# Kernel optimization log

Hardware: AMD Instinct MI355X
Metric: run time of the kernel (lower is better)

Reference implementation:

```python
import jax, jax.numpy as jnp
import numpy as np

C = 512
GROUPS = 32
EPS = 1e-6


def setup_inputs() -> dict:
    key = jax.random.key(0)
    ks = jax.random.split(key, 10)
    B, H, W = 4, 64, 64
    s = 1.0 / np.sqrt(C)
    return {
        "x": jax.random.normal(ks[0], (B, C, H, W), dtype=jnp.float32),
        "gn_weight": jnp.ones((C,), jnp.float32),
        "gn_bias": jnp.zeros((C,), jnp.float32),
        "Wq": jax.random.normal(ks[1], (C, C), jnp.float32) * s,
        "bq": jnp.zeros((C,), jnp.float32),
        "Wk": jax.random.normal(ks[2], (C, C), jnp.float32) * s,
        "bk": jnp.zeros((C,), jnp.float32),
        "Wv": jax.random.normal(ks[3], (C, C), jnp.float32) * s,
        "bv": jnp.zeros((C,), jnp.float32),
        "Wo": jax.random.normal(ks[4], (C, C), jnp.float32) * s,
        "bo": jnp.zeros((C,), jnp.float32),
    }


def _group_norm(x, weight, bias):
    B, Ch, H, W = x.shape
    xg = x.reshape(B, GROUPS, Ch // GROUPS, H, W)
    mean = jnp.mean(xg, axis=(2, 3, 4), keepdims=True)
    var = jnp.var(xg, axis=(2, 3, 4), keepdims=True)
    xg = (xg - mean) * jax.lax.rsqrt(var + EPS)
    h = xg.reshape(B, Ch, H, W)
    return h * weight[None, :, None, None] + bias[None, :, None, None]


def reference(x, gn_weight, gn_bias, Wq, bq, Wk, bk, Wv, bv, Wo, bo):
    B, Ch, H, W = x.shape
    h = _group_norm(x, gn_weight, gn_bias)
    # [B, N, C] with N = H*W spatial tokens
    h = h.reshape(B, Ch, H * W).transpose(0, 2, 1)
    q = h @ Wq.T + bq
    k = h @ Wk.T + bk
    v = h @ Wv.T + bv
    scale = 1.0 / jnp.sqrt(jnp.asarray(Ch, x.dtype))
    scores = jnp.einsum("bnc,bmc->bnm", q, k) * scale  # [B, N, N]
    attn = jax.nn.softmax(scores, axis=-1)
    out = jnp.einsum("bnm,bmc->bnc", attn, v)
    out = out @ Wo.T + bo  # Dropout(0.0) is identity
    out = out.transpose(0, 2, 1).reshape(B, Ch, H, W)
    return x + out
```

## Files before the change

kernel.cpp:

```cpp
#include <hip/hip_runtime.h>
#include <hip/hip_bf16.h>

typedef __attribute__((ext_vector_type(8))) short bf16x8;
typedef __attribute__((ext_vector_type(4))) short bf16x4;
typedef __attribute__((ext_vector_type(4))) float f32x4;

__device__ __forceinline__ short f2bf(float f){
  __hip_bfloat16 h = __float2bfloat16(f);
  return __builtin_bit_cast(short, h);
}
__device__ __forceinline__ float bf2f(short s){
  unsigned u = ((unsigned)(unsigned short)s) << 16;
  return __builtin_bit_cast(float, u);
}

__device__ __forceinline__ void gload_lds16(const short* g, char* l){
  __builtin_amdgcn_global_load_lds(
      (const __attribute__((address_space(1))) void*)g,
      (__attribute__((address_space(3))) void*)l, 16, 0, 0);
}

#define SB0() __builtin_amdgcn_sched_barrier(0)

__global__ __launch_bounds__(256) void gn_stats(const float* __restrict__ x,
                                                float* __restrict__ stats){
  int b = blockIdx.x >> 5, g = blockIdx.x & 31;
  const float4* p = (const float4*)(x + ((long long)b*512 + g*16)*4096);
  float s = 0.f, s2 = 0.f;
  for (int i = threadIdx.x; i < 16384; i += 256){
    float4 v = p[i];
    s  += v.x + v.y + v.z + v.w;
    s2 += v.x*v.x + v.y*v.y + v.z*v.z + v.w*v.w;
  }
  #pragma unroll
  for (int o = 32; o; o >>= 1){ s += __shfl_xor(s, o); s2 += __shfl_xor(s2, o); }
  __shared__ float rs[4], rs2[4];
  int wid = threadIdx.x >> 6;
  if ((threadIdx.x & 63) == 0){ rs[wid] = s; rs2[wid] = s2; }
  __syncthreads();
  if (threadIdx.x == 0){
    float S  = rs[0]+rs[1]+rs[2]+rs[3];
    float S2 = rs2[0]+rs2[1]+rs2[2]+rs2[3];
    float mean = S * (1.f/65536.f);
    float var  = S2 * (1.f/65536.f) - mean*mean;
    stats[blockIdx.x*2]   = mean;
    stats[blockIdx.x*2+1] = rsqrtf(var + 1e-6f);
  }
}

__global__ __launch_bounds__(256) void gn_apply(const float* __restrict__ x,
                                                const float* __restrict__ stats,
                                                const float* __restrict__ gw,
                                                const float* __restrict__ gb,
                                                short* __restrict__ h){
  __shared__ float tile[128][65];
  int b  = blockIdx.y;
  int n0 = blockIdx.x * 64;
  int t  = threadIdx.x;
  const float* xb = x + (long long)b*512*4096;
  for (int cc = 0; cc < 4; cc++){
    int c0 = cc*128;
    #pragma unroll
    for (int r = 0; r < 128; r += 4){
      int c = r + (t >> 6);
      tile[c][t & 63] = xb[(long long)(c0+c)*4096 + n0 + (t & 63)];
    }
    __syncthreads();
    int n = t >> 2, cp = (t & 3)*32;
    short tmp[32];
    #pragma unroll
    for (int j = 0; j < 32; j++){
      int c = c0 + cp + j;
      float mean = stats[(b*32 + (c >> 4))*2];
      float rstd = stats[(b*32 + (c >> 4))*2 + 1];
      float v = (tile[cp+j][n] - mean)*rstd*gw[c] + gb[c];
      tmp[j] = f2bf(v);
    }
    long long ho = ((long long)b*4096 + n0 + n)*512 + c0 + cp;
    #pragma unroll
    for (int j2 = 0; j2 < 4; j2++){
      bf16x8 v8;
      #pragma unroll
      for (int e = 0; e < 8; e++) v8[e] = tmp[j2*8 + e];
      *(bf16x8*)&h[ho + j2*8] = v8;
    }
    __syncthreads();
  }
}

__global__ __launch_bounds__(256) void f2bf_all(
    const float* __restrict__ w0, const float* __restrict__ w1,
    const float* __restrict__ w2, const float* __restrict__ w3,
    short* __restrict__ o0, short* __restrict__ o1,
    short* __restrict__ o2, short* __restrict__ o3){
  int idx = blockIdx.x*256 + threadIdx.x;
  int m = idx >> 15, r = idx & 32767;
  const float* src = (m==0) ? w0 : (m==1) ? w1 : (m==2) ? w2 : w3;
  short* dst       = (m==0) ? o0 : (m==1) ? o1 : (m==2) ? o2 : o3;
  const float4* p = (const float4*)src + (long long)r*2;
  float4 a = p[0], c = p[1];
  bf16x8 v;
  v[0]=f2bf(a.x); v[1]=f2bf(a.y); v[2]=f2bf(a.z); v[3]=f2bf(a.w);
  v[4]=f2bf(c.x); v[5]=f2bf(c.y); v[6]=f2bf(c.z); v[7]=f2bf(c.w);
  *(bf16x8*)&dst[(long long)r*8] = v;
}

__global__ __launch_bounds__(256) void bcat(const float* __restrict__ bq,
                                            const float* __restrict__ bk,
                                            const float* __restrict__ bv,
                                            float* __restrict__ o){
  int t = blockIdx.x*256 + threadIdx.x;
  if (t < 512){ o[t] = bq[t]; o[512+t] = bk[t]; o[1024+t] = bv[t]; }
}

__global__ __launch_bounds__(256) void reduce_den(const float* __restrict__ partial,
                                                  float* __restrict__ inv_den,
                                                  int nrows){
  int r = blockIdx.x*256 + threadIdx.x;
  if (r >= nrows) return;
  const float4* p = (const float4*)(partial + (long long)r*16);
  float4 a = p[0], b = p[1], c = p[2], d = p[3];
  float s = a.x+a.y+a.z+a.w + b.x+b.y+b.z+b.w + c.x+c.y+c.z+c.w + d.x+d.y+d.z+d.w;
  inv_den[r] = 1.f / s;
}

__global__ __launch_bounds__(512, 2) void gemm8(
    const short* __restrict__ A, const short* __restrict__ Bw,
    short* __restrict__ outp,
    int Nn, int Kd,
    long long sA, long long sB, long long sO,
    float* __restrict__ partial)
{
  constexpr int BUFSZ = 65536;
  extern __shared__ char smem[];

  int id = blockIdx.x;
  int xcd = id & 7, s = id >> 3;
  int region = xcd + ((s >> 4) << 3);
  int o = s & 15;
  const int bz = region >> 4;
  const int bx = (region & 3)*4 + (o & 3);
  const int by = ((region >> 2) & 3)*4 + (o >> 2);

  const short* Ab = A + bz*sA;
  const short* Bb = Bw + bz*sB;
  const int m0 = bx*256, n0 = by*256;
  const int t = threadIdx.x;
  const int lane = t & 63, wid = t >> 6;
  const int g = lane >> 4, lr = lane & 15;
  const int wr = wid >> 2, wc = wid & 3;
  const long long KdLL = Kd;

  auto STG = [&](int kt, int buf, int which){
    const bool isB = which >= 2;
    const int h = which & 1;
    char* d = smem + buf*BUFSZ + (isB ? 32768 : 0) + h*16384 + t*16;
    const short* src = isB ? Bb : Ab;
    const int base = isB ? n0 : m0;
    #pragma unroll
    for (int p = 0; p < 2; p++){
      int row = h*128 + p*64 + (t >> 3);
      int ch = t & 7;
      gload_lds16(src + (long long)(base+row)*KdLL + (long long)kt*64 + ((ch ^ (row&7))*8),
                  d + p*8192);
    }
  };

  int roA[8], swA[8], roB[4], swB[4];
  #pragma unroll
  for (int mf = 0; mf < 8; mf++){
    int ra = wr*128 + mf*16 + lr;
    roA[mf] = ra*128; swA[mf] = ra & 7;
  }
  #pragma unroll
  for (int nf = 0; nf < 4; nf++){
    int rb = wc*64 + nf*16 + lr;
    roB[nf] = 32768 + rb*128; swB[nf] = rb & 7;
  }

  f32x4 acc[8][4];
  #pragma unroll
  for (int i = 0; i < 8; i++)
    #pragma unroll
    for (int j = 0; j < 4; j++)
      acc[i][j] = f32x4{0.f,0.f,0.f,0.f};

  bf16x8 av[4][2], bv[4][2];

  #define RD_A(QM, BASE)                                                   \
    _Pragma("unroll")                                                      \
    for (int _i = 0; _i < 4; _i++)                                         \
      _Pragma("unroll")                                                    \
      for (int _ks = 0; _ks < 2; _ks++)                                    \
        av[_i][_ks] = *(const bf16x8*)((BASE) + roA[(QM)*4+_i] +           \
                       (((_ks*4+g) ^ swA[(QM)*4+_i])<<4));
  #define RD_B(QN, BASE)                                                   \
    _Pragma("unroll")                                                      \
    for (int _j = 0; _j < 2; _j++)                                         \
      _Pragma("unroll")                                                    \
      for (int _ks = 0; _ks < 2; _ks++)                                    \
        bv[(QN)*2+_j][_ks] = *(const bf16x8*)((BASE) + roB[(QN)*2+_j] +    \
                       (((_ks*4+g) ^ swB[(QN)*2+_j])<<4));
  #define MFMA16(QN)                                                       \
    __builtin_amdgcn_s_setprio(1);                                         \
    _Pragma("unroll")                                                      \
    for (int _ks = 0; _ks < 2; _ks++)                                      \
      _Pragma("unroll")                                                    \
      for (int _m = 0; _m < 4; _m++)                                       \
        _Pragma("unroll")                                                  \
        for (int _j = 0; _j < 2; _j++)                                     \
          accp[_m][(QN)*2+_j] = __builtin_amdgcn_mfma_f32_16x16x32_bf16(   \
            bv[(QN)*2+_j][_ks], av[_m][_ks], accp[_m][(QN)*2+_j], 0,0,0);  \
    __builtin_amdgcn_s_setprio(0);

  #define LGKM0() asm volatile("s_waitcnt lgkmcnt(0)" ::: "memory")
  #define LGKM8() asm volatile("s_waitcnt lgkmcnt(8)" ::: "memory")
  #define VM4()   asm volatile("s_waitcnt vmcnt(4)" ::: "memory")
  #define VM0()   asm volatile("s_waitcnt vmcnt(0)" ::: "memory")
  #define BAR()   __builtin_amdgcn_s_barrier()

  const int NT = Kd >> 6;
  const int NI = NT >> 1;

  STG(0,0,0); STG(0,0,1); STG(0,0,2); STG(0,0,3);
  STG(1,1,2); STG(1,1,3);
  VM4();
  BAR();

  for (int i = 0; i < NI; ++i){
    const int kt0 = 2*i, kt1 = kt0 + 1;
    char* bc = smem + (kt0 & 1)*BUFSZ;
    char* bn = smem + (kt1 & 1)*BUFSZ;
    {
      f32x4 (&accp)[8][4] = acc;
      RD_A(0, bc); RD_B(0, bc);
      if (kt1 < NT) STG(kt1, kt1 & 1, 0);
      LGKM8();
      BAR();
      LGKM0();
      { f32x4 (&accp2)[8][4] = acc; (void)accp2; }
      __builtin_amdgcn_s_setprio(1);
      #pragma unroll
      for (int _ks = 0; _ks < 2; _ks++)
        #pragma unroll
        for (int _m = 0; _m < 4; _m++)
          #pragma unroll
          for (int _j = 0; _j < 2; _j++)
            acc[_m][_j] = __builtin_amdgcn_mfma_f32_16x16x32_bf16(
              bv[_j][_ks], av[_m][_ks], acc[_m][_j], 0,0,0);
      __builtin_amdgcn_s_setprio(0);
      BAR();
      RD_B(1, bc);
      if (kt1 < NT) STG(kt1, kt1 & 1, 1);
      BAR();
      LGKM0();
      __builtin_amdgcn_s_setprio(1);
      #pragma unroll
      for (int _ks = 0; _ks < 2; _ks++)
        #pragma unroll
        for (int _m = 0; _m < 4; _m++)
          #pragma unroll
          for (int _j = 2; _j < 4; _j++)
            acc[_m][_j] = __builtin_amdgcn_mfma_f32_16x16x32_bf16(
              bv[_j][_ks], av[_m][_ks], acc[_m][_j], 0,0,0);
      __builtin_amdgcn_s_setprio(0);
      BAR();
      RD_A(1, bc);
      if (kt0+2 < NT) STG(kt0+2, kt0 & 1, 2);
      BAR();
      LGKM0();
      __builtin_amdgcn_s_setprio(1);
      #pragma unroll
      for (int _ks = 0; _ks < 2; _ks++)
        #pragma unroll
        for (int _m = 0; _m < 4; _m++)
          #pragma unroll
          for (int _j = 0; _j < 2; _j++)
            acc[4+_m][_j] = __builtin_amdgcn_mfma_f32_16x16x32_bf16(
              bv[_j][_ks], av[_m][_ks], acc[4+_m][_j], 0,0,0);
      __builtin_amdgcn_s_setprio(0);
      BAR();
      if (kt0+2 < NT) STG(kt0+2, kt0 & 1, 3);
      BAR();
      __builtin_amdgcn_s_setprio(1);
      #pragma unroll
      for (int _ks = 0; _ks < 2; _ks++)
        #pragma unroll
        for (int _m = 0; _m < 4; _m++)
          #pragma unroll
          for (int _j = 2; _j < 4; _j++)
            acc[4+_m][_j] = __builtin_amdgcn_mfma_f32_16x16x32_bf16(
              bv[_j][_ks], av[_m][_ks], acc[4+_m][_j], 0,0,0);
      __builtin_amdgcn_s_setprio(0);
      if (kt1 < NT) VM4(); else VM0();
      BAR();
    }
    if (kt1 < NT){
      RD_A(0, bn); RD_B(0, bn);
      if (kt0+2 < NT) STG(kt0+2, kt0 & 1, 0);
      LGKM8();
      BAR();
      LGKM0();
      __builtin_amdgcn_s_setprio(1);
      #pragma unroll
      for (int _ks = 0; _ks < 2; _ks++)
        #pragma unroll
        for (int _m = 0; _m < 4; _m++)
          #pragma unroll
          for (int _j = 0; _j < 2; _j++)
            acc[_m][_j] = __builtin_amdgcn_mfma_f32_16x16x32_bf16(
              bv[_j][_ks], av[_m][_ks], acc[_m][_j], 0,0,0);
      __builtin_amdgcn_s_setprio(0);
      BAR();
      RD_B(1, bn);
      if (kt0+2 < NT) STG(kt0+2, kt0 & 1, 1);
      BAR();
      LGKM0();
      __builtin_amdgcn_s_setprio(1);
      #pragma unroll
      for (int _ks = 0; _ks < 2; _ks++)
        #pragma unroll
        for (int _m = 0; _m < 4; _m++)
          #pragma unroll
          for (int _j = 2; _j < 4; _j++)
            acc[_m][_j] = __builtin_amdgcn_mfma_f32_16x16x32_bf16(
              bv[_j][_ks], av[_m][_ks], acc[_m][_j], 0,0,0);
      __builtin_amdgcn_s_setprio(0);
      BAR();
      RD_A(1, bn);
      if (kt1+2 < NT) STG(kt1+2, kt1 & 1, 2);
      BAR();
      LGKM0();
      __builtin_amdgcn_s_setprio(1);
      #pragma unroll
      for (int _ks = 0; _ks < 2; _ks++)
        #pragma unroll
        for (int _m = 0; _m < 4; _m++)
          #pragma unroll
          for (int _j = 0; _j < 2; _j++)
            acc[4+_m][_j] = __builtin_amdgcn_mfma_f32_16x16x32_bf16(
              bv[_j][_ks], av[_m][_ks], acc[4+_m][_j], 0,0,0);
      __builtin_amdgcn_s_setprio(0);
      BAR();
      if (kt1+2 < NT) STG(kt1+2, kt1 & 1, 3);
      BAR();
      __builtin_amdgcn_s_setprio(1);
      #pragma unroll
      for (int _ks = 0; _ks < 2; _ks++)
        #pragma unroll
        for (int _m = 0; _m < 4; _m++)
          #pragma unroll
          for (int _j = 2; _j < 4; _j++)
            acc[4+_m][_j] = __builtin_amdgcn_mfma_f32_16x16x32_bf16(
              bv[_j][_ks], av[_m][_ks], acc[4+_m][_j], 0,0,0);
      __builtin_amdgcn_s_setprio(0);
      if (kt1+2 < NT) VM4(); else VM0();
      BAR();
    }
  }

  short* outb = outp + bz*sO;
  float* rowpart = (float*)smem;
  constexpr float LOG2E = 1.4426950408889634f;
  #pragma unroll
  for (int mi = 0; mi < 8; mi++){
    int lrow = wr*128 + mi*16 + lr;
    int row  = m0 + lrow;
    float rs = 0.f;
    #pragma unroll
    for (int ni = 0; ni < 4; ni++){
      int col = n0 + wc*64 + ni*16 + g*4;
      bf16x4 pk;
      #pragma unroll
      for (int i2 = 0; i2 < 4; i2++){
        float p = exp2f(acc[mi][ni][i2]*LOG2E);
        rs += p;
        pk[i2] = f2bf(p);
      }
      *(bf16x4*)&outb[(long long)row*Nn + col] = pk;
    }
    rs += __shfl_xor(rs, 16);
    rs += __shfl_xor(rs, 32);
    if (g == 0) rowpart[lrow*4 + wc] = rs;
  }
  __syncthreads();
  if (t < 256){
    float s2 = rowpart[t*4] + rowpart[t*4+1] + rowpart[t*4+2] + rowpart[t*4+3];
    partial[((long long)bz*4096 + m0 + t)*16 + by] = s2;
  }
  #undef RD_A
  #undef RD_B
  #undef MFMA16
  #undef LGKM0
  #undef LGKM8
  #undef VM4
  #undef VM0
  #undef BAR
}

template<int MODE, int TM, int BN, int TH, int SWZ>
__global__ __launch_bounds__(TH, 2) void gemmF(
    const short* __restrict__ A, const short* __restrict__ Bw,
    const float* __restrict__ bias,
    void* __restrict__ outp, const float* __restrict__ resid,
    int M, int Nn, int Kd,
    long long sA, long long sB, long long sO, float scale,
    const float* __restrict__ dptr, float* __restrict__ partial)
{
  constexpr int WAVES   = TH/64;
  constexpr int WARPS_N = BN/64;
  constexpr int WARPS_M = WAVES/WARPS_N;
  constexpr int WM = TM/WARPS_M;
  constexpr int MF = WM/16;
  constexpr int ABYT = TM*128;
  constexpr int BUFSZ = (TM+BN)*128;
  constexpr int APASS = (TM*128)/(TH*16);
  constexpr int BPASS = (BN*128)/(TH*16);
  constexpr int LOADS = APASS + BPASS;
  extern __shared__ char smem[];

  int bx, by, bz;
  if constexpr (SWZ == 2){
    int id = blockIdx.x;
    int xcd = id & 7, s = id >> 3;
    int combo = xcd*2 + (s & 1);
    by = combo & 3; bz = combo >> 2;
    bx = s >> 1;
  } else { bx = blockIdx.x; by = blockIdx.y; bz = blockIdx.z; }

  const short* Ab = A + bz*sA;
  const short* Bb = Bw + bz*sB;
  const int m0 = bx*TM, n0 = by*BN;
  const int t = threadIdx.x;
  const int lane = t & 63, wid = t >> 6;
  const int g = lane >> 4, lr = lane & 15;
  const int wr = wid / WARPS_N, wc = wid % WARPS_N;
  const long long KdLL = Kd;

  auto STAGE = [&](int kt, int buf){
    char* d0 = smem + buf*BUFSZ;
    #pragma unroll
    for (int p = 0; p < APASS; p++){
      int f = p*TH*16 + t*16;
      int row = f >> 7, ch = (f >> 4) & 7;
      gload_lds16(Ab + (long long)(m0+row)*KdLL + (long long)kt*64 + ((ch ^ (row&7))*8),
                  d0 + f);
    }
    #pragma unroll
    for (int p = 0; p < BPASS; p++){
      int f = p*TH*16 + t*16;
      int row = f >> 7, ch = (f >> 4) & 7;
      gload_lds16(Bb + (long long)(n0+row)*KdLL + (long long)kt*64 + ((ch ^ (row&7))*8),
                  d0 + ABYT + f);
    }
  };

  int roA[MF], swA[MF], roB[4], swB[4];
  #pragma unroll
  for (int mf = 0; mf < MF; mf++){
    int ra = wr*WM + mf*16 + lr;
    roA[mf] = ra*128; swA[mf] = ra & 7;
  }
  #pragma unroll
  for (int nf = 0; nf < 4; nf++){
    int rb = wc*64 + nf*16 + lr;
    roB[nf] = ABYT + rb*128; swB[nf] = rb & 7;
  }

  f32x4 acc[MF][4];
  #pragma unroll
  for (int i = 0; i < MF; i++)
    #pragma unroll
    for (int j = 0; j < 4; j++)
      acc[i][j] = f32x4{0.f,0.f,0.f,0.f};

  const int NT = Kd >> 6;

  STAGE(0, 0);
  STAGE(1, 1);
  if constexpr (LOADS == 8) asm volatile("s_waitcnt vmcnt(8)":::"memory");
  else                      asm volatile("s_waitcnt vmcnt(6)":::"memory");
  SB0();
  __builtin_amdgcn_s_barrier();

  for (int kt = 0; kt < NT; ++kt){
    char* base = smem + (kt & 1)*BUFSZ;
    bf16x8 av[MF][2], bv[4][2];
    #pragma unroll
    for (int n = 0; n < 4; n++)
      #pragma unroll
      for (int ks = 0; ks < 2; ks++)
        bv[n][ks] = *(const bf16x8*)(base + roB[n] + (((ks*4+g) ^ swB[n])<<4));
    #pragma unroll
    for (int m = 0; m < MF; m++)
      #pragma unroll
      for (int ks = 0; ks < 2; ks++)
        av[m][ks] = *(const bf16x8*)(base + roA[m] + (((ks*4+g) ^ swA[m])<<4));
    #pragma unroll
    for (int ks = 0; ks < 2; ks++)
      #pragma unroll
      for (int m = 0; m < MF; m++)
        #pragma unroll
        for (int n = 0; n < 4; n++){
          if constexpr (MODE == 2)
            acc[m][n] = __builtin_amdgcn_mfma_f32_16x16x32_bf16(av[m][ks], bv[n][ks], acc[m][n], 0,0,0);
          else
            acc[m][n] = __builtin_amdgcn_mfma_f32_16x16x32_bf16(bv[n][ks], av[m][ks], acc[m][n], 0,0,0);
        }
    SB0();
    __builtin_amdgcn_s_barrier();
    SB0();
    if (kt + 2 < NT){
      STAGE(kt + 2, kt & 1);
      if constexpr (LOADS == 8) asm volatile("s_waitcnt vmcnt(8)":::"memory");
      else                      asm volatile("s_waitcnt vmcnt(6)":::"memory");
    } else {
      asm volatile("s_waitcnt vmcnt(0)":::"memory");
    }
    __builtin_amdgcn_s_barrier();
  }

  if constexpr (MODE == 4){
    short* outb = (short*)outp + bz*sO;
    float* rowpart = (float*)smem;
    constexpr float LOG2E = 1.4426950408889634f;
    #pragma unroll
    for (int mi = 0; mi < MF; mi++){
      int lrow = wr*WM + mi*16 + lr;
      int row  = m0 + lrow;
      float rs = 0.f;
      #pragma unroll
      for (int ni = 0; ni < 4; ni++){
        int col = n0 + wc*64 + ni*16 + g*4;
        bf16x4 pk;
        #pragma unroll
        for (int i = 0; i < 4; i++){
          float p = exp2f(acc[mi][ni][i]*LOG2E);
          rs += p;
          pk[i] = f2bf(p);
        }
        *(bf16x4*)&outb[(long long)row*Nn + col] = pk;
      }
      rs += __shfl_xor(rs, 16);
      rs += __shfl_xor(rs, 32);
      if (g == 0) rowpart[lrow*WARPS_N + wc] = rs;
    }
    __syncthreads();
    if (t < TM){
      float s2 = 0.f;
      #pragma unroll
      for (int j = 0; j < WARPS_N; j++) s2 += rowpart[t*WARPS_N + j];
      partial[((long long)bz*4096 + m0 + t)*16 + by] = s2;
    }
  } else if constexpr (MODE == 5){
    short* outb = (short*)outp + bz*sO;
    const float* dd = dptr + (long long)bz*M;
    #pragma unroll
    for (int mi = 0; mi < MF; mi++){
      int row = m0 + wr*WM + mi*16 + lr;
      float inv = dd[row];
      #pragma unroll
      for (int ni = 0; ni < 4; ni++){
        int col = n0 + wc*64 + ni*16 + g*4;
        bf16x4 pk;
        #pragma unroll
        for (int i = 0; i < 4; i++) pk[i] = f2bf(acc[mi][ni][i]*inv);
        *(bf16x4*)&outb[(long long)row*Nn + col] = pk;
      }
    }
  } else if constexpr (MODE == 6){
    const int seg = by >> 2;
    const long long base = (long long)bz*sO;
    short* qp  = (short*)outp;
    short* kp  = (short*)partial;
    short* vtp = (short*)dptr;
    #pragma unroll
    for (int mi = 0; mi < MF; mi++){
      int row = m0 + wr*WM + mi*16 + lr;
      #pragma unroll
      for (int ni = 0; ni < 4; ni++){
        int col = n0 + wc*64 + ni*16 + g*4;
        float4 bb = *(const float4*)&bias[col];
        int cq = col - seg*512;
        float sc = (seg == 0) ? scale : 1.f;
        bf16x4 pk;
        pk[0] = f2bf((acc[mi][ni][0] + bb.x)*sc);
        pk[1] = f2bf((acc[mi][ni][1] + bb.y)*sc);
        pk[2] = f2bf((acc[mi][ni][2] + bb.z)*sc);
        pk[3] = f2bf((acc[mi][ni][3] + bb.w)*sc);
        if (seg == 0)      *(bf16x4*)&qp[base + (long long)row*512 + cq] = pk;
        else if (seg == 1) *(bf16x4*)&kp[base + (long long)row*512 + cq] = pk;
        else {
          #pragma unroll
          for (int i = 0; i < 4; i++)
            vtp[base + (long long)(cq+i)*4096 + row] = pk[i];
        }
      }
    }
  } else {
    float* outb = (float*)outp + bz*sO;
    const float* rx = resid + bz*sO;
    #pragma unroll
    for (int ni = 0; ni < 4; ni++){
      int col = n0 + wc*64 + ni*16 + lr;
      float bv2 = bias[col];
      #pragma unroll
      for (int mi = 0; mi < MF; mi++){
        int row = m0 + wr*WM + mi*16 + g*4;
        long long off = (long long)col*M + row;
        float4 xr = *(const float4*)&rx[off];
        float4 o;
        o.x = acc[mi][ni][0] + bv2 + xr.x;
        o.y = acc[mi][ni][1] + bv2 + xr.y;
        o.z = acc[mi][ni][2] + bv2 + xr.z;
        o.w = acc[mi][ni][3] + bv2 + xr.w;
        *(float4*)&outb[off] = o;
      }
    }
  }
}

extern "C" void kernel_launch(void* const* d_in, const int* in_sizes, int n_in,
                              void* d_out, int out_size, void* d_ws, size_t ws_size,
                              hipStream_t stream)
{
  const float* x   = (const float*)d_in[0];
  const float* gnw = (const float*)d_in[1];
  const float* gnb = (const float*)d_in[2];
  const float* Wq  = (const float*)d_in[3];
  const float* bq  = (const float*)d_in[4];
  const float* Wk  = (const float*)d_in[5];
  const float* bk  = (const float*)d_in[6];
  const float* Wv  = (const float*)d_in[7];
  const float* bvp = (const float*)d_in[8];
  const float* Wo  = (const float*)d_in[9];
  const float* bo  = (const float*)d_in[10];
  float* out = (float*)d_out;

  char* ws = (char*)d_ws;
  const size_t MB = 1ull << 20;
  short* h      = (short*)(ws);
  short* q      = (short*)(ws + 16*MB);
  short* kmat   = (short*)(ws + 32*MB);
  short* vt     = (short*)(ws + 48*MB);
  short* ao     = (short*)(ws + 64*MB);
  short* wqkv   = (short*)(ws + 80*MB);
  short* wob    = wqkv + 3*262144;
  float* stats  = (float*)(ws + 82*MB);
  float* inv_den= (float*)(ws + 82*MB + 8192);
  float* bqkv   = (float*)(ws + 82*MB + 131072);
  float* partial= (float*)(ws + 83*MB);
  short* S      = (short*)(ws + 84*MB);

  const int LDS_8P = 131072;
  const int LDS_SC = 131072;
  const int LDS_QK = 98304;
  const int LDS_PV = 65536;
  hipFuncSetAttribute(reinterpret_cast<const void*>(&gemm8),
                      hipFuncAttributeMaxDynamicSharedMemorySize, LDS_8P);
  hipFuncSetAttribute(reinterpret_cast<const void*>(&gemmF<4,256,256,512,0>),
                      hipFuncAttributeMaxDynamicSharedMemorySize, LDS_SC);
  hipFuncSetAttribute(reinterpret_cast<const void*>(&gemmF<6,256,128,512,0>),
                      hipFuncAttributeMaxDynamicSharedMemorySize, LDS_QK);
  hipFuncSetAttribute(reinterpret_cast<const void*>(&gemmF<5,128,128,256,2>),
                      hipFuncAttributeMaxDynamicSharedMemorySize, LDS_PV);
  hipFuncSetAttribute(reinterpret_cast<const void*>(&gemmF<5,128,128,256,0>),
                      hipFuncAttributeMaxDynamicSharedMemorySize, LDS_PV);
  hipFuncSetAttribute(reinterpret_cast<const void*>(&gemmF<2,128,128,256,0>),
                      hipFuncAttributeMaxDynamicSharedMemorySize, LDS_PV);

  dim3 blk(256);
  dim3 blk512(512);
  gn_stats<<<dim3(128), blk, 0, stream>>>(x, stats);
  gn_apply<<<dim3(64,4), blk, 0, stream>>>(x, stats, gnw, gnb, h);
  f2bf_all<<<dim3(512), blk, 0, stream>>>(Wq, Wk, Wv, Wo, wqkv, wqkv + 262144, wqkv + 2*262144, wob);
  bcat<<<dim3(2), blk, 0, stream>>>(bq, bk, bvp, bqkv);

  const long long sTok = 4096ll*512;
  const long long sS   = 4096ll*4096;
  const float qscale = 0.044194173824159216f;

  gemmF<6,256,128,512,0><<<dim3(16,12,4), blk512, LDS_QK, stream>>>(
      h, wqkv, bqkv, q, nullptr, 4096, 1536, 512, sTok, 0, sTok, qscale,
      (const float*)vt, (float*)kmat);

  if (ws_size >= 212*MB){
    gemm8<<<dim3(1024), blk512, LDS_8P, stream>>>(
        q, kmat, S, 4096, 512, sTok, sTok, sS, partial);
    reduce_den<<<dim3(64), blk, 0, stream>>>(partial, inv_den, 16384);
    gemmF<5,128,128,256,2><<<dim3(512), blk, LDS_PV, stream>>>(
        S, vt, nullptr, ao, nullptr, 4096, 512, 4096, sS, sTok, sTok, 1.f, inv_den, nullptr);
  } else {
    for (int b = 0; b < 4; b++){
      gemmF<4,256,256,512,0><<<dim3(16,16,1), blk512, LDS_SC, stream>>>(
          q + b*sTok, kmat + b*sTok, nullptr, S, nullptr, 4096, 4096, 512, 0, 0, 0, 1.f, nullptr, partial);
      reduce_den<<<dim3(16), blk, 0, stream>>>(partial, inv_den, 4096);
      gemmF<5,128,128,256,0><<<dim3(32,4,1), blk, LDS_PV, stream>>>(
          S, vt + b*sTok, nullptr, ao + b*sTok, nullptr, 4096, 512, 4096, 0, 0, 0, 1.f, inv_den, nullptr);
    }
  }

  gemmF<2,128,128,256,0><<<dim3(32,4,4), blk, LDS_PV, stream>>>(
      ao, wob, bo, out, x, 4096, 512, 512, sTok, 0, sTok, 1.f, nullptr, nullptr);
}
```

Baseline: 295.5 us.

## Make QK^T exp kernel persistent over four tiles and enlarge PV/out-proj tiles

The scores kernel now launches 256 blocks that each loop over four 256x256 output tiles. The next tile's first K-slices are prefetched into LDS while the current tile's exp/store epilogue runs, and the row-sum scratch moves to a separate LDS region so it cannot collide with the prefetch. The PV and output-projection GEMMs switch from 128x128 tiles with 256 threads to 256x128 tiles with 512 threads, and the PV kernel gets a new XCD-aware block swizzle. The aim is to hide epilogue and launch tail cost and to improve reuse per block, at the cost of fewer blocks and lower occupancy flexibility.

After: 332.9 us. +12.7%, slower.

```diff
diff --git a/kernel.cpp b/kernel.cpp
--- a/kernel.cpp
+++ b/kernel.cpp
@@ -124,7 +124,7 @@
   inv_den[r] = 1.f / s;
 }
 
-__global__ __launch_bounds__(512, 2) void gemm8(
+__global__ __launch_bounds__(512, 2) void gemm8p(
     const short* __restrict__ A, const short* __restrict__ Bw,
     short* __restrict__ outp,
     int Nn, int Kd,
@@ -133,23 +133,28 @@
 {
   constexpr int BUFSZ = 65536;
   extern __shared__ char smem[];
+  float* rowpart = (float*)(smem + 131072);
 
   int id = blockIdx.x;
-  int xcd = id & 7, s = id >> 3;
-  int region = xcd + ((s >> 4) << 3);
-  int o = s & 15;
+  int xcd = id & 7, s2 = id >> 3;
+  int region = xcd + ((s2 >> 2) << 3);
+  int q = s2 & 3;
   const int bz = region >> 4;
-  const int bx = (region & 3)*4 + (o & 3);
-  const int by = ((region >> 2) & 3)*4 + (o >> 2);
-
-  const short* Ab = A + bz*sA;
-  const short* Bb = Bw + bz*sB;
-  const int m0 = bx*256, n0 = by*256;
+
   const int t = threadIdx.x;
   const int lane = t & 63, wid = t >> 6;
   const int g = lane >> 4, lr = lane & 15;
   const int wr = wid >> 2, wc = wid & 3;
   const long long KdLL = Kd;
+
+  const short* Ab; const short* Bb; int m0, n0;
+  auto SETTILE = [&](int j){
+    int o = q*4 + j;
+    int bx = (region & 3)*4 + (o & 3);
+    int by = ((region >> 2) & 3)*4 + (o >> 2);
+    m0 = bx*256; n0 = by*256;
+    Ab = A + bz*sA; Bb = Bw + bz*sB;
+  };
 
   auto STG = [&](int kt, int buf, int which){
     const bool isB = which >= 2;
@@ -201,16 +206,16 @@
       for (int _ks = 0; _ks < 2; _ks++)                                    \
         bv[(QN)*2+_j][_ks] = *(const bf16x8*)((BASE) + roB[(QN)*2+_j] +    \
                        (((_ks*4+g) ^ swB[(QN)*2+_j])<<4));
-  #define MFMA16(QN)                                                       \
+  #define MFMAQ(MB, J0)                                                    \
     __builtin_amdgcn_s_setprio(1);                                         \
     _Pragma("unroll")                                                      \
     for (int _ks = 0; _ks < 2; _ks++)                                      \
       _Pragma("unroll")                                                    \
       for (int _m = 0; _m < 4; _m++)                                       \
         _Pragma("unroll")                                                  \
-        for (int _j = 0; _j < 2; _j++)                                     \
-          accp[_m][(QN)*2+_j] = __builtin_amdgcn_mfma_f32_16x16x32_bf16(   \
-            bv[(QN)*2+_j][_ks], av[_m][_ks], accp[_m][(QN)*2+_j], 0,0,0);  \
+        for (int _j = (J0); _j < (J0)+2; _j++)                             \
+          acc[(MB)+_m][_j] = __builtin_amdgcn_mfma_f32_16x16x32_bf16(      \
+            bv[_j][_ks], av[_m][_ks], acc[(MB)+_m][_j], 0,0,0);            \
     __builtin_amdgcn_s_setprio(0);
 
   #define LGKM0() asm volatile("s_waitcnt lgkmcnt(0)" ::: "memory")
@@ -222,175 +227,120 @@
   const int NT = Kd >> 6;
   const int NI = NT >> 1;
 
+  SETTILE(0);
   STG(0,0,0); STG(0,0,1); STG(0,0,2); STG(0,0,3);
   STG(1,1,2); STG(1,1,3);
   VM4();
   BAR();
 
-  for (int i = 0; i < NI; ++i){
-    const int kt0 = 2*i, kt1 = kt0 + 1;
-    char* bc = smem + (kt0 & 1)*BUFSZ;
-    char* bn = smem + (kt1 & 1)*BUFSZ;
-    {
-      f32x4 (&accp)[8][4] = acc;
+  for (int jt = 0; jt < 4; ++jt){
+    for (int i = 0; i < NI; ++i){
+      const int kt0 = 2*i, kt1 = kt0 + 1;
+      char* bc = smem + (kt0 & 1)*BUFSZ;
+      char* bn = smem + (kt1 & 1)*BUFSZ;
       RD_A(0, bc); RD_B(0, bc);
-      if (kt1 < NT) STG(kt1, kt1 & 1, 0);
+      STG(kt1, kt1 & 1, 0);
       LGKM8();
       BAR();
       LGKM0();
-      { f32x4 (&accp2)[8][4] = acc; (void)accp2; }
-      __builtin_amdgcn_s_setprio(1);
-      #pragma unroll
-      for (int _ks = 0; _ks < 2; _ks++)
-        #pragma unroll
-        for (int _m = 0; _m < 4; _m++)
-          #pragma unroll
-          for (int _j = 0; _j < 2; _j++)
-            acc[_m][_j] = __builtin_amdgcn_mfma_f32_16x16x32_bf16(
-              bv[_j][_ks], av[_m][_ks], acc[_m][_j], 0,0,0);
-      __builtin_amdgcn_s_setprio(0);
+      MFMAQ(0, 0);
       BAR();
       RD_B(1, bc);
-      if (kt1 < NT) STG(kt1, kt1 & 1, 1);
-      BAR();
-      LGKM0();
-      __builtin_amdgcn_s_setprio(1);
-      #pragma unroll
-      for (int _ks = 0; _ks < 2; _ks++)
-        #pragma unroll
-        for (int _m = 0; _m < 4; _m++)
-          #pragma unroll
-          for (int _j = 2; _j < 4; _j++)
-            acc[_m][_j] = __builtin_amdgcn_mfma_f32_16x16x32_bf16(
-              bv[_j][_ks], av[_m][_ks], acc[_m][_j], 0,0,0);
-      __builtin_amdgcn_s_setprio(0);
+      STG(kt1, kt1 & 1, 1);
+      BAR();
+      LGKM0();
+      MFMAQ(0, 2);
       BAR();
       RD_A(1, bc);
       if (kt0+2 < NT) STG(kt0+2, kt0 & 1, 2);
       BAR();
       LGKM0();
-      __builtin_amdgcn_s_setprio(1);
-      #pragma unroll
-      for (int _ks = 0; _ks < 2; _ks++)
-        #pragma unroll
-        for (int _m = 0; _m < 4; _m++)
-          #pragma unroll
-          for (int _j = 0; _j < 2; _j++)
-            acc[4+_m][_j] = __builtin_amdgcn_mfma_f32_16x16x32_bf16(
-              bv[_j][_ks], av[_m][_ks], acc[4+_m][_j], 0,0,0);
-      __builtin_amdgcn_s_setprio(0);
+      MFMAQ(4, 0);
       BAR();
       if (kt0+2 < NT) STG(kt0+2, kt0 & 1, 3);
       BAR();
-      __builtin_amdgcn_s_setprio(1);
-      #pragma unroll
-      for (int _ks = 0; _ks < 2; _ks++)
-        #pragma unroll
-        for (int _m = 0; _m < 4; _m++)
-          #pragma unroll
-          for (int _j = 2; _j < 4; _j++)
-            acc[4+_m][_j] = __builtin_amdgcn_mfma_f32_16x16x32_bf16(
-              bv[_j][_ks], av[_m][_ks], acc[4+_m][_j], 0,0,0);
-      __builtin_amdgcn_s_setprio(0);
-      if (kt1 < NT) VM4(); else VM0();
-      BAR();
-    }
-    if (kt1 < NT){
+      MFMAQ(4, 2);
+      VM4();
+      BAR();
       RD_A(0, bn); RD_B(0, bn);
       if (kt0+2 < NT) STG(kt0+2, kt0 & 1, 0);
       LGKM8();
       BAR();
       LGKM0();
-      __builtin_amdgcn_s_setprio(1);
-      #pragma unroll
-      for (int _ks = 0; _ks < 2; _ks++)
-        #pragma unroll
-        for (int _m = 0; _m < 4; _m++)
-          #pragma unroll
-          for (int _j = 0; _j < 2; _j++)
-            acc[_m][_j] = __builtin_amdgcn_mfma_f32_16x16x32_bf16(
-              bv[_j][_ks], av[_m][_ks], acc[_m][_j], 0,0,0);
-      __builtin_amdgcn_s_setprio(0);
+      MFMAQ(0, 0);
       BAR();
       RD_B(1, bn);
       if (kt0+2 < NT) STG(kt0+2, kt0 & 1, 1);
       BAR();
       LGKM0();
-      __builtin_amdgcn_s_setprio(1);
-      #pragma unroll
-      for (int _ks = 0; _ks < 2; _ks++)
-        #pragma unroll
-        for (int _m = 0; _m < 4; _m++)
-          #pragma unroll
-          for (int _j = 2; _j < 4; _j++)
-            acc[_m][_j] = __builtin_amdgcn_mfma_f32_16x16x32_bf16(
-              bv[_j][_ks], av[_m][_ks], acc[_m][_j], 0,0,0);
-      __builtin_amdgcn_s_setprio(0);
+      MFMAQ(0, 2);
       BAR();
       RD_A(1, bn);
       if (kt1+2 < NT) STG(kt1+2, kt1 & 1, 2);
       BAR();
       LGKM0();
-      __builtin_amdgcn_s_setprio(1);
-      #pragma unroll
-      for (int _ks = 0; _ks < 2; _ks++)
+      MFMAQ(4, 0);
+      BAR();
+      if (kt1+2 < NT) STG(kt1+2, kt1 & 1, 3);
+      BAR();
+      MFMAQ(4, 2);
+      if (kt1+2 < NT) VM4(); else VM0();
+      BAR();
+    }
+
+    const int pm0 = m0, pn0 = n0, pby = n0 >> 8;
+    if (jt < 3){
+      SETTILE(jt + 1);
+      STG(0,0,0); STG(0,0,1); STG(0,0,2); STG(0,0,3);
+      STG(1,1,2); STG(1,1,3);
+    }
+
+    {
+      short* outb = outp + bz*sO;
+      constexpr float LOG2E = 1.4426950408889634f;
+      #pragma unroll
+      for (int mi = 0; mi < 8; mi++){
+        int lrow = wr*128 + mi*16 + lr;
+        int row  = pm0 + lrow;
+        float rs = 0.f;
         #pragma unroll
-        for (int _m = 0; _m < 4; _m++)
+        for (int ni = 0; ni < 4; ni++){
+          int col = pn0 + wc*64 + ni*16 + g*4;
+          bf16x4 pk;
           #pragma unroll
-          for (int _j = 0; _j < 2; _j++)
-            acc[4+_m][_j] = __builtin_amdgcn_mfma_f32_16x16x32_bf16(
-              bv[_j][_ks], av[_m][_ks], acc[4+_m][_j], 0,0,0);
-      __builtin_amdgcn_s_setprio(0);
-      BAR();
-      if (kt1+2 < NT) STG(kt1+2, kt1 & 1, 3);
-      BAR();
-      __builtin_amdgcn_s_setprio(1);
-      #pragma unroll
-      for (int _ks = 0; _ks < 2; _ks++)
-        #pragma unroll
-        for (int _m = 0; _m < 4; _m++)
-          #pragma unroll
-          for (int _j = 2; _j < 4; _j++)
-            acc[4+_m][_j] = __builtin_amdgcn_mfma_f32_16x16x32_bf16(
-              bv[_j][_ks], av[_m][_ks], acc[4+_m][_j], 0,0,0);
-      __builtin_amdgcn_s_setprio(0);
-      if (kt1+2 < NT) VM4(); else VM0();
-      BAR();
-    }
-  }
-
-  short* outb = outp + bz*sO;
-  float* rowpart = (float*)smem;
-  constexpr float LOG2E = 1.4426950408889634f;
-  #pragma unroll
-  for (int mi = 0; mi < 8; mi++){
-    int lrow = wr*128 + mi*16 + lr;
-    int row  = m0 + lrow;
-    float rs = 0.f;
-    #pragma unroll
-    for (int ni = 0; ni < 4; ni++){
-      int col = n0 + wc*64 + ni*16 + g*4;
-      bf16x4 pk;
-      #pragma unroll
-      for (int i2 = 0; i2 < 4; i2++){
-        float p = exp2f(acc[mi][ni][i2]*LOG2E);
-        rs += p;
-        pk[i2] = f2bf(p);
+          for (int i2 = 0; i2 < 4; i2++){
+            float p = exp2f(acc[mi][ni][i2]*LOG2E);
+            rs += p;
+            pk[i2] = f2bf(p);
+          }
+          *(bf16x4*)&outb[(long long)row*Nn + col] = pk;
+        }
+        rs += __shfl_xor(rs, 16);
+        rs += __shfl_xor(rs, 32);
+        if (g == 0) rowpart[lrow*4 + wc] = rs;
       }
-      *(bf16x4*)&outb[(long long)row*Nn + col] = pk;
-    }
-    rs += __shfl_xor(rs, 16);
-    rs += __shfl_xor(rs, 32);
-    if (g == 0) rowpart[lrow*4 + wc] = rs;
-  }
-  __syncthreads();
-  if (t < 256){
-    float s2 = rowpart[t*4] + rowpart[t*4+1] + rowpart[t*4+2] + rowpart[t*4+3];
-    partial[((long long)bz*4096 + m0 + t)*16 + by] = s2;
+      LGKM0();
+      BAR();
+      if (t < 256){
+        float s3 = rowpart[t*4] + rowpart[t*4+1] + rowpart[t*4+2] + rowpart[t*4+3];
+        partial[((long long)bz*4096 + pm0 + t)*16 + pby] = s3;
+      }
+      LGKM0();
+      BAR();
+    }
+    #pragma unroll
+    for (int i = 0; i < 8; i++)
+      #pragma unroll
+      for (int j = 0; j < 4; j++)
+        acc[i][j] = f32x4{0.f,0.f,0.f,0.f};
+    if (jt < 3){
+      VM4();
+      BAR();
+    }
   }
   #undef RD_A
   #undef RD_B
-  #undef MFMA16
+  #undef MFMAQ
   #undef LGKM0
   #undef LGKM8
   #undef VM4
@@ -420,12 +370,13 @@
   extern __shared__ char smem[];
 
   int bx, by, bz;
-  if constexpr (SWZ == 2){
+  if constexpr (SWZ == 3){
     int id = blockIdx.x;
     int xcd = id & 7, s = id >> 3;
-    int combo = xcd*2 + (s & 1);
-    by = combo & 3; bz = combo >> 2;
-    bx = s >> 1;
+    bx = xcd*2 + (s & 1);
+    int rem = s >> 1;
+    int nby = Nn / BN;
+    by = rem % nby; bz = rem / nby;
   } else { bx = blockIdx.x; by = blockIdx.y; bz = blockIdx.z; }
 
   const short* Ab = A + bz*sA;
@@ -652,22 +603,22 @@
   float* partial= (float*)(ws + 83*MB);
   short* S      = (short*)(ws + 84*MB);
 
-  const int LDS_8P = 131072;
+  const int LDS_8P = 135168;
   const int LDS_SC = 131072;
   const int LDS_QK = 98304;
-  const int LDS_PV = 65536;
-  hipFuncSetAttribute(reinterpret_cast<const void*>(&gemm8),
+  const int LDS_BIG = 98304;
+  hipFuncSetAttribute(reinterpret_cast<const void*>(&gemm8p),
                       hipFuncAttributeMaxDynamicSharedMemorySize, LDS_8P);
   hipFuncSetAttribute(reinterpret_cast<const void*>(&gemmF<4,256,256,512,0>),
                       hipFuncAttributeMaxDynamicSharedMemorySize, LDS_SC);
   hipFuncSetAttribute(reinterpret_cast<const void*>(&gemmF<6,256,128,512,0>),
                       hipFuncAttributeMaxDynamicSharedMemorySize, LDS_QK);
-  hipFuncSetAttribute(reinterpret_cast<const void*>(&gemmF<5,128,128,256,2>),
-                      hipFuncAttributeMaxDynamicSharedMemorySize, LDS_PV);
-  hipFuncSetAttribute(reinterpret_cast<const void*>(&gemmF<5,128,128,256,0>),
-                      hipFuncAttributeMaxDynamicSharedMemorySize, LDS_PV);
-  hipFuncSetAttribute(reinterpret_cast<const void*>(&gemmF<2,128,128,256,0>),
-                      hipFuncAttributeMaxDynamicSharedMemorySize, LDS_PV);
+  hipFuncSetAttribute(reinterpret_cast<const void*>(&gemmF<5,256,128,512,3>),
+                      hipFuncAttributeMaxDynamicSharedMemorySize, LDS_BIG);
+  hipFuncSetAttribute(reinterpret_cast<const void*>(&gemmF<5,256,128,512,0>),
+                      hipFuncAttributeMaxDynamicSharedMemorySize, LDS_BIG);
+  hipFuncSetAttribute(reinterpret_cast<const void*>(&gemmF<2,256,128,512,0>),
+                      hipFuncAttributeMaxDynamicSharedMemorySize, LDS_BIG);
 
   dim3 blk(256);
   dim3 blk512(512);
@@ -685,21 +636,21 @@
       (const float*)vt, (float*)kmat);
 
   if (ws_size >= 212*MB){
-    gemm8<<<dim3(1024), blk512, LDS_8P, stream>>>(
+    gemm8p<<<dim3(256), blk512, LDS_8P, stream>>>(
         q, kmat, S, 4096, 512, sTok, sTok, sS, partial);
     reduce_den<<<dim3(64), blk, 0, stream>>>(partial, inv_den, 16384);
-    gemmF<5,128,128,256,2><<<dim3(512), blk, LDS_PV, stream>>>(
+    gemmF<5,256,128,512,3><<<dim3(256), blk512, LDS_BIG, stream>>>(
         S, vt, nullptr, ao, nullptr, 4096, 512, 4096, sS, sTok, sTok, 1.f, inv_den, nullptr);
   } else {
     for (int b = 0; b < 4; b++){
       gemmF<4,256,256,512,0><<<dim3(16,16,1), blk512, LDS_SC, stream>>>(
           q + b*sTok, kmat + b*sTok, nullptr, S, nullptr, 4096, 4096, 512, 0, 0, 0, 1.f, nullptr, partial);
       reduce_den<<<dim3(16), blk, 0, stream>>>(partial, inv_den, 4096);
-      gemmF<5,128,128,256,0><<<dim3(32,4,1), blk, LDS_PV, stream>>>(
+      gemmF<5,256,128,512,0><<<dim3(16,4,1), blk512, LDS_BIG, stream>>>(
           S, vt + b*sTok, nullptr, ao + b*sTok, nullptr, 4096, 512, 4096, 0, 0, 0, 1.f, inv_den, nullptr);
     }
   }
 
-  gemmF<2,128,128,256,0><<<dim3(32,4,4), blk, LDS_PV, stream>>>(
+  gemmF<2,256,128,512,0><<<dim3(16,4,4), blk512, LDS_BIG, stream>>>(
       ao, wob, bo, out, x, 4096, 512, 512, sTok, 0, sTok, 1.f, nullptr, nullptr);
 }
```
